# Kernel optimization log

Hardware: AMD Instinct MI355X
Metric: run time of the kernel (lower is better)

Reference implementation:

```python
import jax, jax.numpy as jnp
import numpy as np

B = 131072
EPS = 1e-5

def _attn(x, Wq, Wk, Wv, Wo):
    # x: (B, 10, 1); Wq/Wk/Wv: (1, 16); Wo: (16, 1)
    Q = x @ Wq  # (B, 10, 16)
    K = x @ Wk
    V = x @ Wv
    A = jnp.einsum('bqd,bkd->bqk', Q, K) / 4.0  # sqrt(16) = 4
    A = jax.nn.softmax(A, axis=1)  # NOTE: torch Softmax(dim=1) -> axis 1, not -1
    out = jnp.einsum('bqk,bkd->bqd', A, V) @ Wo  # (B, 10, 1)
    return out[..., 0]  # squeeze -> (B, 10)

def _bn(h, gamma, beta):
    # BatchNorm1d training-mode math (batch stats, biased variance)
    mu = jnp.mean(h, axis=0)
    var = jnp.mean(jnp.square(h - mu), axis=0)
    return gamma * (h - mu) * jax.lax.rsqrt(var + EPS) + beta

def setup_inputs() -> dict:
    key = jax.random.key(0)
    ks = jax.random.split(key, 24)
    n = lambda k, shp, s=1.0: (jax.random.normal(k, shp, dtype=jnp.float32) * s)
    inp = {
        'x':   n(ks[0], (B, 10, 1)),
        'Wq1': n(ks[1], (1, 16)), 'Wk1': n(ks[2], (1, 16)),
        'Wv1': n(ks[3], (1, 16)), 'Wo1': n(ks[4], (16, 1)),
        'Wq2': n(ks[5], (1, 16)), 'Wk2': n(ks[6], (1, 16)),
        'Wv2': n(ks[7], (1, 16)), 'Wo2': n(ks[8], (16, 1)),
        # layer1: Linear(10,128) BN ReLU Linear(128,256) BN ReLU Linear(256,10)
        'W1a': n(ks[9], (10, 128), 0.3), 'b1a': jnp.zeros((128,), jnp.float32),
        'g1a': jnp.ones((128,), jnp.float32), 'be1a': jnp.zeros((128,), jnp.float32),
        'W1b': n(ks[10], (128, 256), 0.09), 'b1b': jnp.zeros((256,), jnp.float32),
        'g1b': jnp.ones((256,), jnp.float32), 'be1b': jnp.zeros((256,), jnp.float32),
        'W1c': n(ks[11], (256, 10), 0.06), 'b1c': jnp.zeros((10,), jnp.float32),
        # layer2: Linear(10,128) BN ReLU Linear(128,256) BN ReLU Linear(256,2)
        'W2a': n(ks[12], (10, 128), 0.3), 'b2a': jnp.zeros((128,), jnp.float32),
        'g2a': jnp.ones((128,), jnp.float32), 'be2a': jnp.zeros((128,), jnp.float32),
        'W2b': n(ks[13], (128, 256), 0.09), 'b2b': jnp.zeros((256,), jnp.float32),
        'g2b': jnp.ones((256,), jnp.float32), 'be2b': jnp.zeros((256,), jnp.float32),
        'W2c': n(ks[14], (256, 2), 0.06), 'b2c': jnp.zeros((2,), jnp.float32),
    }
    return inp

def reference(x, Wq1, Wk1, Wv1, Wo1, Wq2, Wk2, Wv2, Wo2,
              W1a, b1a, g1a, be1a, W1b, b1b, g1b, be1b, W1c, b1c,
              W2a, b2a, g2a, be2a, W2b, b2b, g2b, be2b, W2c, b2c):
    h = _attn(x, Wq1, Wk1, Wv1, Wo1)                 # (B, 10)
    h = jax.nn.relu(_bn(h @ W1a + b1a, g1a, be1a))   # (B, 128)
    h = jax.nn.relu(_bn(h @ W1b + b1b, g1b, be1b))   # (B, 256)
    h = h @ W1c + b1c                                # (B, 10)
    h = _attn(h[..., None], Wq2, Wk2, Wv2, Wo2)      # (B, 10)
    h = jax.nn.relu(_bn(h @ W2a + b2a, g2a, be2a))   # (B, 128)
    h = jax.nn.relu(_bn(h @ W2b + b2b, g2b, be2b))   # (B, 256)
    return h @ W2c + b2c                             # (B, 2)
```

## Files before the change

kernel.cpp:

```cpp
#include <hip/hip_runtime.h>
#include <hip/hip_bf16.h>

#define EPS 1e-5f
constexpr int BN = 131072;
constexpr int NBKT = 32;
constexpr int NTILE = BN/64;
constexpr int TILE_ELEMS = 256*64;

typedef __attribute__((ext_vector_type(8))) short bf16x8;
typedef __attribute__((ext_vector_type(4))) float f32x4;

constexpr size_t OFF_H   = 0;
constexpr size_t OFF_HH  = OFF_H  + (size_t)BN*10;
constexpr size_t OFF_M1  = OFF_HH + (size_t)BN*10;
constexpr size_t OFF_S2  = OFF_M1 + 65;
constexpr size_t OFF_M3  = OFF_S2 + 512;
constexpr size_t OFF_S4  = OFF_M3 + 65;
constexpr size_t OFF_WA1 = OFF_S4 + 512;
constexpr size_t OFF_BA1 = OFF_WA1 + 1280;
constexpr size_t OFF_WA2 = OFF_BA1 + 128;
constexpr size_t OFF_BA2 = OFF_WA2 + 1280;
constexpr size_t OFF_SC2 = OFF_BA2 + 128;
constexpr size_t OFF_TC2 = OFF_SC2 + 256;
constexpr size_t OFF_SC4 = OFF_TC2 + 256;
constexpr size_t OFF_TC4 = OFF_SC4 + 256;
constexpr size_t OFF_WB1 = OFF_TC4 + 256;
constexpr size_t OFF_BB1 = OFF_WB1 + 32768;
constexpr size_t OFF_WB2 = OFF_BB1 + 256;
constexpr size_t OFF_BB2 = OFF_WB2 + 32768;
constexpr size_t OFF_P1  = OFF_BB2 + 256;
constexpr size_t OFF_P3  = OFF_P1 + 1024*65;
constexpr size_t OFF_S2B = OFF_P3 + 1024*65;
constexpr size_t OFF_S4B = OFF_S2B + (size_t)NBKT*512;
constexpr size_t OFF_WT1 = OFF_S4B + (size_t)NBKT*512;
constexpr size_t OFF_WT2 = OFF_WT1 + 16384;
constexpr size_t OFF_END = OFF_WT2 + 16384;
constexpr size_t OFF_Z_BYTES = ((OFF_END*4 + 255) & ~(size_t)255);
constexpr size_t WS_NEED = OFF_Z_BYTES + (size_t)NTILE*TILE_ELEMS*2;

__device__ __forceinline__ float wsum(float v){
  v += __shfl_down(v, 32);
  v += __shfl_down(v, 16);
  v += __shfl_down(v, 8);
  v += __shfl_down(v, 4);
  v += __shfl_down(v, 2);
  v += __shfl_down(v, 1);
  return v;
}

__device__ __forceinline__ unsigned pk_bf16(float a, float b){
  union { __hip_bfloat16 h[2]; unsigned u; } cv;
  cv.h[0] = __float2bfloat16(a);
  cv.h[1] = __float2bfloat16(b);
  return cv.u;
}

__device__ __forceinline__ unsigned short bf16_1(float a){
  union { __hip_bfloat16 h; unsigned short u; } cv;
  cv.h = __float2bfloat16(a);
  return cv.u;
}

__device__ __forceinline__ float bf16_to_f(unsigned short u){
  return __uint_as_float(((unsigned)u) << 16);
}

__device__ __forceinline__ void attn10(const float* xr, float cqk, float cvo, float* y){
  #pragma unroll
  for (int q=0;q<10;q++) y[q] = 0.f;
  #pragma unroll
  for (int k=0;k<10;k++){
    float t = cqk * xr[k];
    float m = t*xr[0];
    #pragma unroll
    for (int q=1;q<10;q++) m = fmaxf(m, t*xr[q]);
    float ex[10]; float s = 0.f;
    #pragma unroll
    for (int q=0;q<10;q++){ ex[q] = __expf(t*xr[q]-m); s += ex[q]; }
    float f = xr[k]/s;
    #pragma unroll
    for (int q=0;q<10;q++) y[q] += ex[q]*f;
  }
  #pragma unroll
  for (int q=0;q<10;q++) y[q] *= cvo;
}

__device__ __forceinline__ void moments_block(const float* y, float (*red)[65],
                                              float* Pb, int t){
  int lane = t & 63, w = t >> 6;
  #pragma unroll
  for (int i=0;i<10;i++){
    float v = wsum(y[i]);
    if (lane==0) red[w][i] = v;
  }
  #pragma unroll
  for (int i=0;i<10;i++){
    #pragma unroll
    for (int j=i;j<10;j++){
      float v = wsum(y[i]*y[j]);
      if (lane==0) red[w][10 + 10*i - i*(i-1)/2 + (j-i)] = v;
    }
  }
  __syncthreads();
  if (t < 65)
    Pb[(size_t)blockIdx.x*65 + t] = red[0][t]+red[1][t]+red[2][t]+red[3][t];
}

__device__ __forceinline__ void moments10(const float* y, float* M, int lane){
  #pragma unroll
  for (int i=0;i<10;i++){
    float s = wsum(y[i]);
    if (lane==0) atomicAdd(&M[i], s);
  }
  #pragma unroll
  for (int i=0;i<10;i++){
    #pragma unroll
    for (int j=i;j<10;j++){
      int id = 10*i - i*(i-1)/2 + (j-i);
      float s = wsum(y[i]*y[j]);
      if (lane==0) atomicAdd(&M[10+id], s);
    }
  }
}

__global__ __launch_bounds__(256) void k_attn_in(
    const float* __restrict__ x,
    const float* __restrict__ Wq, const float* __restrict__ Wk,
    const float* __restrict__ Wv, const float* __restrict__ Wo,
    float* __restrict__ h, float* __restrict__ Pb){
  __shared__ float xs[256][11];
  __shared__ float red[4][65];
  int t = threadIdx.x;
  size_t base = (size_t)blockIdx.x*2560;
  for (int idx=t; idx<2560; idx+=256) xs[idx/10][idx%10] = x[base+idx];
  float cqk=0.f, cvo=0.f;
  #pragma unroll
  for (int d=0;d<16;d++){ cqk += Wq[d]*Wk[d]; cvo += Wv[d]*Wo[d]; }
  cqk *= 0.25f;
  __syncthreads();
  float xr[10];
  #pragma unroll
  for (int q=0;q<10;q++) xr[q] = xs[t][q];
  float y[10];
  attn10(xr, cqk, cvo, y);
  #pragma unroll
  for (int q=0;q<10;q++) xs[t][q] = y[q];
  moments_block(y, red, Pb, t);
  for (int idx=t; idx<2560; idx+=256) h[base+idx] = xs[idx/10][idx%10];
}

__global__ void k_fold10_part(const float* __restrict__ Pb, int npart,
                              const float* __restrict__ W,
                              const float* __restrict__ bv, const float* __restrict__ g,
                              const float* __restrict__ be,
                              float* __restrict__ WT, float* __restrict__ bo){
  __shared__ float part[65][8];
  __shared__ float sM[65];
  int t = threadIdx.x;
  if (t < 520){
    int c = t>>3, k = t&7;
    int n = npart>>3;
    float acc = 0.f;
    #pragma unroll 4
    for (int i=0;i<n;i++) acc += Pb[(size_t)(k*n+i)*65 + c];
    part[c][k] = acc;
  }
  __syncthreads();
  if (t < 65){
    float a = 0.f;
    #pragma unroll
    for (int k=0;k<8;k++) a += part[t][k];
    sM[t] = a;
  }
  __syncthreads();
  int j = t;
  if (j >= 128) return;
  const float invB = 1.f/(float)BN;
  float Eh[10];
  #pragma unroll
  for (int i=0;i<10;i++) Eh[i] = sM[i]*invB;
  float wj[10];
  #pragma unroll
  for (int i=0;i<10;i++) wj[i] = W[i*128+j];
  float mu = bv[j];
  #pragma unroll
  for (int i=0;i<10;i++) mu += Eh[i]*wj[i];
  float var = 0.f;
  #pragma unroll
  for (int i=0;i<10;i++){
    #pragma unroll
    for (int l=0;l<10;l++){
      int a = i<l ? i : l, c = i<l ? l : i;
      int id = 10*a - a*(a-1)/2 + (c-a);
      float cov = sM[10+id]*invB - Eh[i]*Eh[l];
      var += wj[i]*wj[l]*cov;
    }
  }
  float s = g[j]*rsqrtf(var + EPS);
  #pragma unroll
  for (int i=0;i<10;i++) WT[j*10+i] = wj[i]*s;
  bo[j] = (bv[j]-mu)*s + be[j];
}

__global__ void k_fold10_atomic(const float* __restrict__ M,
                                const float* __restrict__ W,
                                const float* __restrict__ bv, const float* __restrict__ g,
                                const float* __restrict__ be,
                                float* __restrict__ WT, float* __restrict__ bo){
  int j = threadIdx.x;
  if (j >= 128) return;
  const float invB = 1.f/(float)BN;
  float Eh[10];
  #pragma unroll
  for (int i=0;i<10;i++) Eh[i] = M[i]*invB;
  float wj[10];
  #pragma unroll
  for (int i=0;i<10;i++) wj[i] = W[i*128+j];
  float mu = bv[j];
  #pragma unroll
  for (int i=0;i<10;i++) mu += Eh[i]*wj[i];
  float var = 0.f;
  #pragma unroll
  for (int i=0;i<10;i++){
    #pragma unroll
    for (int l=0;l<10;l++){
      int a = i<l ? i : l, c = i<l ? l : i;
      int id = 10*a - a*(a-1)/2 + (c-a);
      float cov = M[10+id]*invB - Eh[i]*Eh[l];
      var += wj[i]*wj[l]*cov;
    }
  }
  float s = g[j]*rsqrtf(var + EPS);
  #pragma unroll
  for (int i=0;i<10;i++) WT[j*10+i] = wj[i]*s;
  bo[j] = (bv[j]-mu)*s + be[j];
}

__global__ void k_fold_affine(const float* __restrict__ stats,
                              const float* __restrict__ g,
                              const float* __restrict__ be,
                              float* __restrict__ s, float* __restrict__ tt){
  int j = threadIdx.x;
  if (j >= 256) return;
  float su = 0.f, sq = 0.f;
  #pragma unroll 4
  for (int k=0;k<NBKT;k++){
    su += stats[k*512 + j];
    sq += stats[k*512 + 256 + j];
  }
  const float invB = 1.f/(float)BN;
  float mu  = su*invB;
  float var = sq*invB - mu*mu;
  float sc = g[j]*rsqrtf(var + EPS);
  s[j]  = sc;
  tt[j] = be[j] - mu*sc;
}

__global__ __launch_bounds__(256) void k_prep_wt2(
    const float* __restrict__ W1, const float* __restrict__ W2,
    unsigned short* __restrict__ WT1, unsigned short* __restrict__ WT2){
  int g = blockIdx.x;
  const float* W = (g < 128) ? W1 : W2;
  unsigned short* WT = (g < 128) ? WT1 : WT2;
  int idx = (g & 127)*256 + threadIdx.x;
  int c = idx >> 7, k = idx & 127;
  WT[idx] = bf16_1(W[k*256 + c]);
}

__global__ __launch_bounds__(256) void k_layer_mfma(
    const float* __restrict__ h,
    const float* __restrict__ WaT,
    const float* __restrict__ ba,
    const unsigned short* __restrict__ WT,
    const float* __restrict__ bb,
    unsigned short* __restrict__ zt,
    float* __restrict__ stats)
{
  __shared__ unsigned short h1s[2][64*128];
  __shared__ float hs[128][11];
  __shared__ float sWaT[1280];
  int t = threadIdx.x;
  int lane = t & 63, w = t >> 6;
  int ci = lane & 15, g = lane >> 4;
  size_t row0 = (size_t)blockIdx.x * 128;

  bf16x8 bfr[4][4];
  #pragma unroll
  for (int nt=0; nt<4; nt++)
    #pragma unroll
    for (int kt=0; kt<4; kt++){
      union { uint4 u; bf16x8 v; } cv;
      cv.u = *(const uint4*)(WT + (size_t)(w*64 + nt*16 + ci)*128 + kt*32 + g*8);
      bfr[nt][kt] = cv.v;
    }

  for (int idx = t; idx < 1280; idx += 256) hs[idx/10][idx%10] = h[row0*10 + idx];
  for (int idx = t; idx < 1280; idx += 256) sWaT[idx] = WaT[idx];
  __syncthreads();

  float bbv[4];
  #pragma unroll
  for (int nt=0;nt<4;nt++) bbv[nt] = bb[w*64 + nt*16 + ci];
  float cs[4] = {0,0,0,0}, cq[4] = {0,0,0,0};

  {
    int r = lane;
    int i0 = w * 32;
    float hr[10];
    #pragma unroll
    for (int l=0;l<10;l++) hr[l] = hs[r][l];
    #pragma unroll
    for (int j=0;j<4;j++){
      unsigned pk[4];
      #pragma unroll
      for (int q=0;q<4;q++){
        int i = i0 + j*8 + q*2;
        float v0 = ba[i], v1 = ba[i+1];
        #pragma unroll
        for (int l=0;l<10;l++){
          v0 = fmaf(hr[l], sWaT[i*10+l],     v0);
          v1 = fmaf(hr[l], sWaT[(i+1)*10+l], v1);
        }
        pk[q] = pk_bf16(fmaxf(v0,0.f), fmaxf(v1,0.f));
      }
      int byte = r*256 + (((i0 + j*8)*2) ^ ((r&7)<<4));
      *(uint4*)((char*)h1s[0] + byte) = make_uint4(pk[0],pk[1],pk[2],pk[3]);
    }
  }
  __syncthreads();

  f32x4 acc[4][4];
  #pragma unroll
  for (int mt=0;mt<4;mt++)
    #pragma unroll
    for (int nt=0;nt<4;nt++)
      acc[mt][nt] = (f32x4){0.f,0.f,0.f,0.f};
  #pragma unroll
  for (int mt=0; mt<4; mt++){
    int r = mt*16 + ci;
    bf16x8 af[4];
    #pragma unroll
    for (int kt=0; kt<4; kt++){
      int byte = r*256 + ((kt*64 + g*16) ^ ((r&7)<<4));
      af[kt] = *(const bf16x8*)((const char*)h1s[0] + byte);
    }
    #pragma unroll
    for (int nt=0; nt<4; nt++)
      #pragma unroll
      for (int kt=0; kt<4; kt++)
        acc[mt][nt] = __builtin_amdgcn_mfma_f32_16x16x32_bf16(
            af[kt], bfr[nt][kt], acc[mt][nt], 0, 0, 0);
  }

  {
    size_t tbase = ((size_t)blockIdx.x*2 + 0) * TILE_ELEMS;
    #pragma unroll
    for (int nt=0; nt<4; nt++){
      int c = w*64 + nt*16 + ci;
      #pragma unroll
      for (int mt=0; mt<4; mt++){
        float z0 = acc[mt][nt][0] + bbv[nt];
        float z1 = acc[mt][nt][1] + bbv[nt];
        float z2 = acc[mt][nt][2] + bbv[nt];
        float z3 = acc[mt][nt][3] + bbv[nt];
        cs[nt] += z0+z1+z2+z3;
        cq[nt] += z0*z0+z1*z1+z2*z2+z3*z3;
        *(uint2*)(zt + tbase + c*64 + mt*16 + g*4) =
            make_uint2(pk_bf16(z0,z1), pk_bf16(z2,z3));
      }
    }
  }

  {
    int r = lane;
    int i0 = w * 32;
    float hr[10];
    #pragma unroll
    for (int l=0;l<10;l++) hr[l] = hs[64 + r][l];
    #pragma unroll
    for (int j=0;j<4;j++){
      unsigned pk[4];
      #pragma unroll
      for (int q=0;q<4;q++){
        int i = i0 + j*8 + q*2;
        float v0 = ba[i], v1 = ba[i+1];
        #pragma unroll
        for (int l=0;l<10;l++){
          v0 = fmaf(hr[l], sWaT[i*10+l],     v0);
          v1 = fmaf(hr[l], sWaT[(i+1)*10+l], v1);
        }
        pk[q] = pk_bf16(fmaxf(v0,0.f), fmaxf(v1,0.f));
      }
      int byte = r*256 + (((i0 + j*8)*2) ^ ((r&7)<<4));
      *(uint4*)((char*)h1s[1] + byte) = make_uint4(pk[0],pk[1],pk[2],pk[3]);
    }
  }
  __syncthreads();

  #pragma unroll
  for (int mt=0;mt<4;mt++)
    #pragma unroll
    for (int nt=0;nt<4;nt++)
      acc[mt][nt] = (f32x4){0.f,0.f,0.f,0.f};
  #pragma unroll
  for (int mt=0; mt<4; mt++){
    int r = mt*16 + ci;
    bf16x8 af[4];
    #pragma unroll
    for (int kt=0; kt<4; kt++){
      int byte = r*256 + ((kt*64 + g*16) ^ ((r&7)<<4));
      af[kt] = *(const bf16x8*)((const char*)h1s[1] + byte);
    }
    #pragma unroll
    for (int nt=0; nt<4; nt++)
      #pragma unroll
      for (int kt=0; kt<4; kt++)
        acc[mt][nt] = __builtin_amdgcn_mfma_f32_16x16x32_bf16(
            af[kt], bfr[nt][kt], acc[mt][nt], 0, 0, 0);
  }

  {
    size_t tbase = ((size_t)blockIdx.x*2 + 1) * TILE_ELEMS;
    #pragma unroll
    for (int nt=0; nt<4; nt++){
      int c = w*64 + nt*16 + ci;
      #pragma unroll
      for (int mt=0; mt<4; mt++){
        float z0 = acc[mt][nt][0] + bbv[nt];
        float z1 = acc[mt][nt][1] + bbv[nt];
        float z2 = acc[mt][nt][2] + bbv[nt];
        float z3 = acc[mt][nt][3] + bbv[nt];
        cs[nt] += z0+z1+z2+z3;
        cq[nt] += z0*z0+z1*z1+z2*z2+z3*z3;
        *(uint2*)(zt + tbase + c*64 + mt*16 + g*4) =
            make_uint2(pk_bf16(z0,z1), pk_bf16(z2,z3));
      }
    }
  }

  #pragma unroll
  for (int nt=0; nt<4; nt++){
    float s1 = cs[nt], s2 = cq[nt];
    s1 += __shfl_down(s1, 32); s1 += __shfl_down(s1, 16);
    s2 += __shfl_down(s2, 32); s2 += __shfl_down(s2, 16);
    if (lane < 16){
      int bkt = blockIdx.x & (NBKT-1);
      int c = w*64 + nt*16 + ci;
      atomicAdd(&stats[bkt*512 + c],       s1);
      atomicAdd(&stats[bkt*512 + 256 + c], s2);
    }
  }
}

__global__ __launch_bounds__(256) void k_consume_mid(
    const unsigned short* __restrict__ zt,
    const float* __restrict__ s_g, const float* __restrict__ t_g,
    const float* __restrict__ Wc,  const float* __restrict__ bc,
    const float* __restrict__ Wq, const float* __restrict__ Wk,
    const float* __restrict__ Wv, const float* __restrict__ Wo,
    float* __restrict__ hh, float* __restrict__ Pb){
  __shared__ __align__(16) unsigned short zs[2][32*256];
  __shared__ __align__(16) float sWc[256*12];
  __shared__ float ss[256], st[256];
  __shared__ float red[4][65];
  int t = threadIdx.x;
  for (int idx=t; idx<2560; idx+=256) sWc[(idx/10)*12 + (idx%10)] = Wc[idx];
  ss[t] = s_g[t]; st[t] = t_g[t];
  size_t b0 = (size_t)blockIdx.x*256;

  float z3[10];
  #pragma unroll
  for (int l=0;l<10;l++) z3[l] = bc[l];

  int q = t >> 6, l = t & 63;
  size_t src_base = ((size_t)blockIdx.x*4 + q)*TILE_ELEMS + l*32;
  int dst_off = (l>>1)*256 + q*64 + (l&1)*32;
  uint4 r0, r1, r2, r3;
  {
    const uint4* src = (const uint4*)(zt + src_base);
    r0 = src[0]; r1 = src[1]; r2 = src[2]; r3 = src[3];
    uint4* dst = (uint4*)&zs[0][dst_off];
    dst[0] = r0; dst[1] = r1; dst[2] = r2; dst[3] = r3;
  }
  for (int cc=0; cc<8; cc++){
    __syncthreads();
    if (cc < 7){
      const uint4* src = (const uint4*)(zt + src_base + (size_t)(cc+1)*2048);
      r0 = src[0]; r1 = src[1]; r2 = src[2]; r3 = src[3];
    }
    const unsigned short* zb = zs[cc&1];
    #pragma unroll 4
    for (int cl=0; cl<32; cl++){
      int c = cc*32 + cl;
      float f = bf16_to_f(zb[cl*256 + t]);
      float h2 = fmaxf(fmaf(ss[c], f, st[c]), 0.f);
      const float4* wr = (const float4*)&sWc[c*12];
      float4 w0 = wr[0];
      float4 w1 = wr[1];
      float2 w2 = *(const float2*)&sWc[c*12 + 8];
      z3[0] = fmaf(h2, w0.x, z3[0]); z3[1] = fmaf(h2, w0.y, z3[1]);
      z3[2] = fmaf(h2, w0.z, z3[2]); z3[3] = fmaf(h2, w0.w, z3[3]);
      z3[4] = fmaf(h2, w1.x, z3[4]); z3[5] = fmaf(h2, w1.y, z3[5]);
      z3[6] = fmaf(h2, w1.z, z3[6]); z3[7] = fmaf(h2, w1.w, z3[7]);
      z3[8] = fmaf(h2, w2.x, z3[8]); z3[9] = fmaf(h2, w2.y, z3[9]);
    }
    if (cc < 7){
      uint4* dst = (uint4*)&zs[(cc+1)&1][dst_off];
      dst[0] = r0; dst[1] = r1; dst[2] = r2; dst[3] = r3;
    }
  }

  float cqk=0.f, cvo=0.f;
  #pragma unroll
  for (int d=0;d<16;d++){ cqk += Wq[d]*Wk[d]; cvo += Wv[d]*Wo[d]; }
  cqk *= 0.25f;
  float y[10];
  attn10(z3, cqk, cvo, y);
  __syncthreads();
  float* hhs = (float*)zs[0];
  #pragma unroll
  for (int qq=0;qq<10;qq++) hhs[t*10+qq] = y[qq];
  moments_block(y, red, Pb, t);
  for (int idx=t; idx<2560; idx+=256)
    hh[b0*10 + idx] = hhs[idx];
}

__global__ __launch_bounds__(256) void k_consume_out(
    const unsigned short* __restrict__ zt,
    const float* __restrict__ s_g, const float* __restrict__ t_g,
    const float* __restrict__ Wc,  const float* __restrict__ bc,
    float* __restrict__ out){
  __shared__ __align__(16) unsigned short zs[2][32*256];
  __shared__ __align__(8) float sWo[512];
  __shared__ float ss[256], st[256];
  int t = threadIdx.x;
  sWo[t] = Wc[t]; sWo[256+t] = Wc[256+t];
  ss[t] = s_g[t]; st[t] = t_g[t];
  size_t b0 = (size_t)blockIdx.x*256;
  float o0 = bc[0], o1 = bc[1];
  int q = t >> 6, l = t & 63;
  size_t src_base = ((size_t)blockIdx.x*4 + q)*TILE_ELEMS + l*32;
  int dst_off = (l>>1)*256 + q*64 + (l&1)*32;
  uint4 r0, r1, r2, r3;
  {
    const uint4* src = (const uint4*)(zt + src_base);
    r0 = src[0]; r1 = src[1]; r2 = src[2]; r3 = src[3];
    uint4* dst = (uint4*)&zs[0][dst_off];
    dst[0] = r0; dst[1] = r1; dst[2] = r2; dst[3] = r3;
  }
  for (int cc=0; cc<8; cc++){
    __syncthreads();
    if (cc < 7){
      const uint4* src = (const uint4*)(zt + src_base + (size_t)(cc+1)*2048);
      r0 = src[0]; r1 = src[1]; r2 = src[2]; r3 = src[3];
    }
    const unsigned short* zb = zs[cc&1];
    #pragma unroll 8
    for (int cl=0; cl<32; cl++){
      int c = cc*32 + cl;
      float f = bf16_to_f(zb[cl*256 + t]);
      float h5 = fmaxf(fmaf(ss[c], f, st[c]), 0.f);
      float2 wv = *(const float2*)&sWo[c*2];
      o0 = fmaf(h5, wv.x, o0);
      o1 = fmaf(h5, wv.y, o1);
    }
    if (cc < 7){
      uint4* dst = (uint4*)&zs[(cc+1)&1][dst_off];
      dst[0] = r0; dst[1] = r1; dst[2] = r2; dst[3] = r3;
    }
  }
  *(float2*)(out + (b0 + t)*2) = make_float2(o0, o1);
}

__global__ void k_fold_big(const float* __restrict__ stats,
                           const float* __restrict__ W,
                           const float* __restrict__ bv, const float* __restrict__ g,
                           const float* __restrict__ be,
                           float* __restrict__ Wf, float* __restrict__ bf){
  int j = blockIdx.x*256 + threadIdx.x;
  if (j >= 256) return;
  const float invB = 1.f/(float)BN;
  float mu  = stats[j]*invB;
  float var = stats[256+j]*invB - mu*mu;
  float s = g[j]*rsqrtf(var + EPS);
  bf[j] = (bv[j]-mu)*s + be[j];
  for (int i=0;i<128;i++) Wf[i*256+j] = W[i*256+j]*s;
}

__global__ __launch_bounds__(256) void k_mid(
    const float* __restrict__ h,
    const float* __restrict__ WaT, const float* __restrict__ ba,
    const float* __restrict__ Wb,  const float* __restrict__ bb,
    float* __restrict__ stats){
  int b = blockIdx.x*256 + threadIdx.x;
  if (b >= BN) return;
  float hr[10];
  #pragma unroll
  for (int l=0;l<10;l++) hr[l] = h[(size_t)b*10+l];
  int lane = threadIdx.x & 63;
  for (int jc=0;jc<4;jc++){
    float acc[64];
    #pragma unroll
    for (int j=0;j<64;j++) acc[j] = bb[jc*64+j];
    for (int i=0;i<128;i++){
      float h1 = ba[i];
      #pragma unroll
      for (int l=0;l<10;l++) h1 += hr[l]*WaT[i*10+l];
      h1 = fmaxf(h1, 0.f);
      const float* __restrict__ w = &Wb[i*256 + jc*64];
      #pragma unroll
      for (int j=0;j<64;j++) acc[j] += h1*w[j];
    }
    #pragma unroll
    for (int j=0;j<64;j++){
      float s1 = wsum(acc[j]);
      float s2 = wsum(acc[j]*acc[j]);
      if (lane==0){
        atomicAdd(&stats[jc*64+j], s1);
        atomicAdd(&stats[256+jc*64+j], s2);
      }
    }
  }
}

__global__ __launch_bounds__(256) void k_mid2(
    const float* __restrict__ h,
    const float* __restrict__ WaT, const float* __restrict__ ba,
    const float* __restrict__ Wbf, const float* __restrict__ bbf,
    const float* __restrict__ Wc,  const float* __restrict__ bc,
    const float* __restrict__ Wq, const float* __restrict__ Wk,
    const float* __restrict__ Wv, const float* __restrict__ Wo,
    float* __restrict__ hh, float* __restrict__ M){
  int b = blockIdx.x*256 + threadIdx.x;
  if (b >= BN) return;
  float hr[10];
  #pragma unroll
  for (int l=0;l<10;l++) hr[l] = h[(size_t)b*10+l];
  float z3[10];
  #pragma unroll
  for (int l=0;l<10;l++) z3[l] = bc[l];
  for (int jc=0;jc<4;jc++){
    float acc[64];
    #pragma unroll
    for (int j=0;j<64;j++) acc[j] = bbf[jc*64+j];
    for (int i=0;i<128;i++){
      float h1 = ba[i];
      #pragma unroll
      for (int l=0;l<10;l++) h1 += hr[l]*WaT[i*10+l];
      h1 = fmaxf(h1, 0.f);
      const float* __restrict__ w = &Wbf[i*256 + jc*64];
      #pragma unroll
      for (int j=0;j<64;j++) acc[j] += h1*w[j];
    }
    #pragma unroll
    for (int j=0;j<64;j++){
      float h2 = fmaxf(acc[j], 0.f);
      const float* __restrict__ wc = &Wc[(jc*64+j)*10];
      #pragma unroll
      for (int l=0;l<10;l++) z3[l] += h2*wc[l];
    }
  }
  float cqk=0.f, cvo=0.f;
  #pragma unroll
  for (int d=0;d<16;d++){ cqk += Wq[d]*Wk[d]; cvo += Wv[d]*Wo[d]; }
  cqk *= 0.25f;
  float y[10];
  attn10(z3, cqk, cvo, y);
  #pragma unroll
  for (int q=0;q<10;q++) hh[(size_t)b*10+q] = y[q];
  moments10(y, M, threadIdx.x & 63);
}

__global__ __launch_bounds__(256) void k_out(
    const float* __restrict__ h,
    const float* __restrict__ WaT, const float* __restrict__ ba,
    const float* __restrict__ Wbf, const float* __restrict__ bbf,
    const float* __restrict__ Wc,  const float* __restrict__ bc,
    float* __restrict__ out){
  int b = blockIdx.x*256 + threadIdx.x;
  if (b >= BN) return;
  float hr[10];
  #pragma unroll
  for (int l=0;l<10;l++) hr[l] = h[(size_t)b*10+l];
  float o0 = bc[0], o1 = bc[1];
  for (int jc=0;jc<4;jc++){
    float acc[64];
    #pragma unroll
    for (int j=0;j<64;j++) acc[j] = bbf[jc*64+j];
    for (int i=0;i<128;i++){
      float h4 = ba[i];
      #pragma unroll
      for (int l=0;l<10;l++) h4 += hr[l]*WaT[i*10+l];
      h4 = fmaxf(h4, 0.f);
      const float* __restrict__ w = &Wbf[i*256 + jc*64];
      #pragma unroll
      for (int j=0;j<64;j++) acc[j] += h4*w[j];
    }
    #pragma unroll
    for (int j=0;j<64;j++){
      float h5 = fmaxf(acc[j], 0.f);
      o0 += h5*Wc[(jc*64+j)*2];
      o1 += h5*Wc[(jc*64+j)*2+1];
    }
  }
  out[(size_t)b*2]   = o0;
  out[(size_t)b*2+1] = o1;
}

extern "C" void kernel_launch(void* const* d_in, const int* in_sizes, int n_in,
                              void* d_out, int out_size, void* d_ws, size_t ws_size,
                              hipStream_t stream){
  const float* x   = (const float*)d_in[0];
  const float* Wq1 = (const float*)d_in[1];
  const float* Wk1 = (const float*)d_in[2];
  const float* Wv1 = (const float*)d_in[3];
  const float* Wo1 = (const float*)d_in[4];
  const float* Wq2 = (const float*)d_in[5];
  const float* Wk2 = (const float*)d_in[6];
  const float* Wv2 = (const float*)d_in[7];
  const float* Wo2 = (const float*)d_in[8];
  const float* W1a = (const float*)d_in[9];  const float* b1a = (const float*)d_in[10];
  const float* g1a = (const float*)d_in[11]; const float* be1a= (const float*)d_in[12];
  const float* W1b = (const float*)d_in[13]; const float* b1b = (const float*)d_in[14];
  const float* g1b = (const float*)d_in[15]; const float* be1b= (const float*)d_in[16];
  const float* W1c = (const float*)d_in[17]; const float* b1c = (const float*)d_in[18];
  const float* W2a = (const float*)d_in[19]; const float* b2a = (const float*)d_in[20];
  const float* g2a = (const float*)d_in[21]; const float* be2a= (const float*)d_in[22];
  const float* W2b = (const float*)d_in[23]; const float* b2b = (const float*)d_in[24];
  const float* g2b = (const float*)d_in[25]; const float* be2b= (const float*)d_in[26];
  const float* W2c = (const float*)d_in[27]; const float* b2c = (const float*)d_in[28];

  float* f   = (float*)d_ws;
  float* h   = f + OFF_H;
  float* hh  = f + OFF_HH;
  float* M1  = f + OFF_M1;
  float* S2  = f + OFF_S2;
  float* M3  = f + OFF_M3;
  float* S4  = f + OFF_S4;
  float* WA1 = f + OFF_WA1; float* BA1 = f + OFF_BA1;
  float* WA2 = f + OFF_WA2; float* BA2 = f + OFF_BA2;
  float* SC2 = f + OFF_SC2; float* TC2 = f + OFF_TC2;
  float* SC4 = f + OFF_SC4; float* TC4 = f + OFF_TC4;
  float* WB1 = f + OFF_WB1; float* BB1 = f + OFF_BB1;
  float* WB2 = f + OFF_WB2; float* BB2 = f + OFF_BB2;
  float* P1  = f + OFF_P1;  float* P3  = f + OFF_P3;
  float* S2B = f + OFF_S2B; float* S4B = f + OFF_S4B;
  unsigned short* WT1 = (unsigned short*)(f + OFF_WT1);
  unsigned short* WT2 = (unsigned short*)(f + OFF_WT2);
  unsigned short* ZT = (unsigned short*)((char*)d_ws + OFF_Z_BYTES);

  dim3 blk(256);
  dim3 grid256(BN/256);
  dim3 grid128(BN/128);

  if (ws_size >= WS_NEED){
    hipMemsetAsync(S2B, 0, (size_t)2*NBKT*512*sizeof(float), stream);
    k_prep_wt2<<<256,blk,0,stream>>>(W1b, W2b, WT1, WT2);
    k_attn_in<<<grid256,blk,0,stream>>>(x, Wq1,Wk1,Wv1,Wo1, h, P1);
    k_fold10_part<<<1,576,0,stream>>>(P1, 512, W1a,b1a,g1a,be1a, WA1,BA1);
    k_layer_mfma<<<grid128,blk,0,stream>>>(h, WA1,BA1, WT1,b1b, ZT, S2B);
    k_fold_affine<<<1,256,0,stream>>>(S2B, g1b, be1b, SC2, TC2);
    k_consume_mid<<<grid256,blk,0,stream>>>(ZT, SC2,TC2, W1c,b1c,
                                            Wq2,Wk2,Wv2,Wo2, hh, P3);
    k_fold10_part<<<1,576,0,stream>>>(P3, 512, W2a,b2a,g2a,be2a, WA2,BA2);
    k_layer_mfma<<<grid128,blk,0,stream>>>(hh, WA2,BA2, WT2,b2b, ZT, S4B);
    k_fold_affine<<<1,256,0,stream>>>(S4B, g2b, be2b, SC4, TC4);
    k_consume_out<<<grid256,blk,0,stream>>>(ZT, SC4,TC4, W2c,b2c, (float*)d_out);
  } else {
    hipMemsetAsync(M1, 0, (65+512+65+512)*sizeof(float), stream);
    k_attn_in<<<grid256,blk,0,stream>>>(x, Wq1,Wk1,Wv1,Wo1, h, P1);
    k_fold10_part<<<1,576,0,stream>>>(P1, 512, W1a,b1a,g1a,be1a, WA1,BA1);
    k_mid<<<grid256,blk,0,stream>>>(h, WA1,BA1, W1b,b1b, S2);
    k_fold_big<<<1,256,0,stream>>>(S2, W1b,b1b,g1b,be1b, WB1,BB1);
    k_mid2<<<grid256,blk,0,stream>>>(h, WA1,BA1, WB1,BB1, W1c,b1c,
                                     Wq2,Wk2,Wv2,Wo2, hh, M3);
    k_fold10_atomic<<<1,128,0,stream>>>(M3, W2a,b2a,g2a,be2a, WA2,BA2);
    k_mid<<<grid256,blk,0,stream>>>(hh, WA2,BA2, W2b,b2b, S4);
    k_fold_big<<<1,256,0,stream>>>(S4, W2b,b2b,g2b,be2b, WB2,BB2);
    k_out<<<grid256,blk,0,stream>>>(hh, WA2,BA2, WB2,BB2, W2c,b2c, (float*)d_out);
  }
}
```

Baseline: 207.8 us.

## Process two rows per thread in consume kernels with swizzled single-buffer LDS

The two consumer kernels now handle 512 rows per block, two per thread. Each thread reads a packed pair of bf16 values with one 32-bit LDS load, so the same scale, shift and weight loads serve two rows. The double-buffered staging is replaced by a single XOR-swizzled LDS buffer and eight-vector register prefetch, with an extra barrier per chunk. This halves the grid and changes the partial-moment count passed to the fold kernel, in exchange for more registers per thread and fewer blocks to spread across the device.

```diff
diff --git a/kernel.cpp b/kernel.cpp
--- a/kernel.cpp
+++ b/kernel.cpp
@@ -64,6 +64,8 @@
 __device__ __forceinline__ float bf16_to_f(unsigned short u){
   return __uint_as_float(((unsigned)u) << 16);
 }
+__device__ __forceinline__ float bf16_lo(unsigned u){ return __uint_as_float(u << 16); }
+__device__ __forceinline__ float bf16_hi(unsigned u){ return __uint_as_float(u & 0xffff0000u); }
 
 __device__ __forceinline__ void attn10(const float* xr, float cqk, float cvo, float* y){
   #pragma unroll
@@ -459,54 +461,61 @@
     const float* __restrict__ Wq, const float* __restrict__ Wk,
     const float* __restrict__ Wv, const float* __restrict__ Wo,
     float* __restrict__ hh, float* __restrict__ Pb){
-  __shared__ __align__(16) unsigned short zs[2][32*256];
+  __shared__ __align__(16) unsigned short zs[32*512];
   __shared__ __align__(16) float sWc[256*12];
   __shared__ float ss[256], st[256];
   __shared__ float red[4][65];
   int t = threadIdx.x;
   for (int idx=t; idx<2560; idx+=256) sWc[(idx/10)*12 + (idx%10)] = Wc[idx];
   ss[t] = s_g[t]; st[t] = t_g[t];
-  size_t b0 = (size_t)blockIdx.x*256;
-
-  float z3[10];
-  #pragma unroll
-  for (int l=0;l<10;l++) z3[l] = bc[l];
-
-  int q = t >> 6, l = t & 63;
-  size_t src_base = ((size_t)blockIdx.x*4 + q)*TILE_ELEMS + l*32;
-  int dst_off = (l>>1)*256 + q*64 + (l&1)*32;
-  uint4 r0, r1, r2, r3;
+  size_t b0 = (size_t)blockIdx.x*512;
+
+  float z3a[10], z3b[10];
+  #pragma unroll
+  for (int l=0;l<10;l++){ z3a[l] = bc[l]; z3b[l] = bc[l]; }
+
+  int q8 = t >> 5, cl0 = t & 31;
+  size_t src_base = ((size_t)blockIdx.x*8 + q8)*TILE_ELEMS + (size_t)cl0*64;
+  int sbits = (cl0 & 7) << 4;
+  char* wbase = (char*)zs + cl0*1024;
+
+  uint4 pf[8];
   {
-    const uint4* src = (const uint4*)(zt + src_base);
-    r0 = src[0]; r1 = src[1]; r2 = src[2]; r3 = src[3];
-    uint4* dst = (uint4*)&zs[0][dst_off];
-    dst[0] = r0; dst[1] = r1; dst[2] = r2; dst[3] = r3;
+    const uint4* s = (const uint4*)(zt + src_base);
+    #pragma unroll
+    for (int k=0;k<8;k++) pf[k] = s[k];
   }
   for (int cc=0; cc<8; cc++){
     __syncthreads();
+    #pragma unroll
+    for (int k=0;k<8;k++)
+      *(uint4*)(wbase + ((q8*128 + k*16) ^ sbits)) = pf[k];
     if (cc < 7){
-      const uint4* src = (const uint4*)(zt + src_base + (size_t)(cc+1)*2048);
-      r0 = src[0]; r1 = src[1]; r2 = src[2]; r3 = src[3];
-    }
-    const unsigned short* zb = zs[cc&1];
+      const uint4* s = (const uint4*)(zt + src_base + (size_t)(cc+1)*2048);
+      #pragma unroll
+      for (int k=0;k<8;k++) pf[k] = s[k];
+    }
+    __syncthreads();
     #pragma unroll 4
     for (int cl=0; cl<32; cl++){
       int c = cc*32 + cl;
-      float f = bf16_to_f(zb[cl*256 + t]);
-      float h2 = fmaxf(fmaf(ss[c], f, st[c]), 0.f);
+      unsigned u = *(const unsigned*)((const char*)zs + cl*1024 + ((4*t) ^ ((cl&7)<<4)));
+      float ha = fmaxf(fmaf(ss[c], bf16_lo(u), st[c]), 0.f);
+      float hb = fmaxf(fmaf(ss[c], bf16_hi(u), st[c]), 0.f);
       const float4* wr = (const float4*)&sWc[c*12];
       float4 w0 = wr[0];
       float4 w1 = wr[1];
       float2 w2 = *(const float2*)&sWc[c*12 + 8];
-      z3[0] = fmaf(h2, w0.x, z3[0]); z3[1] = fmaf(h2, w0.y, z3[1]);
-      z3[2] = fmaf(h2, w0.z, z3[2]); z3[3] = fmaf(h2, w0.w, z3[3]);
-      z3[4] = fmaf(h2, w1.x, z3[4]); z3[5] = fmaf(h2, w1.y, z3[5]);
-      z3[6] = fmaf(h2, w1.z, z3[6]); z3[7] = fmaf(h2, w1.w, z3[7]);
-      z3[8] = fmaf(h2, w2.x, z3[8]); z3[9] = fmaf(h2, w2.y, z3[9]);
-    }
-    if (cc < 7){
-      uint4* dst = (uint4*)&zs[(cc+1)&1][dst_off];
-      dst[0] = r0; dst[1] = r1; dst[2] = r2; dst[3] = r3;
+      z3a[0]=fmaf(ha,w0.x,z3a[0]); z3b[0]=fmaf(hb,w0.x,z3b[0]);
+      z3a[1]=fmaf(ha,w0.y,z3a[1]); z3b[1]=fmaf(hb,w0.y,z3b[1]);
+      z3a[2]=fmaf(ha,w0.z,z3a[2]); z3b[2]=fmaf(hb,w0.z,z3b[2]);
+      z3a[3]=fmaf(ha,w0.w,z3a[3]); z3b[3]=fmaf(hb,w0.w,z3b[3]);
+      z3a[4]=fmaf(ha,w1.x,z3a[4]); z3b[4]=fmaf(hb,w1.x,z3b[4]);
+      z3a[5]=fmaf(ha,w1.y,z3a[5]); z3b[5]=fmaf(hb,w1.y,z3b[5]);
+      z3a[6]=fmaf(ha,w1.z,z3a[6]); z3b[6]=fmaf(hb,w1.z,z3b[6]);
+      z3a[7]=fmaf(ha,w1.w,z3a[7]); z3b[7]=fmaf(hb,w1.w,z3b[7]);
+      z3a[8]=fmaf(ha,w2.x,z3a[8]); z3b[8]=fmaf(hb,w2.x,z3b[8]);
+      z3a[9]=fmaf(ha,w2.y,z3a[9]); z3b[9]=fmaf(hb,w2.y,z3b[9]);
     }
   }
 
@@ -514,14 +523,35 @@
   #pragma unroll
   for (int d=0;d<16;d++){ cqk += Wq[d]*Wk[d]; cvo += Wv[d]*Wo[d]; }
   cqk *= 0.25f;
-  float y[10];
-  attn10(z3, cqk, cvo, y);
+  float ya[10], yb[10];
+  attn10(z3a, cqk, cvo, ya);
+  attn10(z3b, cqk, cvo, yb);
+
   __syncthreads();
-  float* hhs = (float*)zs[0];
-  #pragma unroll
-  for (int qq=0;qq<10;qq++) hhs[t*10+qq] = y[qq];
-  moments_block(y, red, Pb, t);
-  for (int idx=t; idx<2560; idx+=256)
+  float* hhs = (float*)zs;
+  #pragma unroll
+  for (int q=0;q<10;q++){ hhs[(2*t)*10+q] = ya[q]; hhs[(2*t+1)*10+q] = yb[q]; }
+
+  {
+    int lane = t & 63, w = t >> 6;
+    #pragma unroll
+    for (int i=0;i<10;i++){
+      float v = wsum(ya[i] + yb[i]);
+      if (lane==0) red[w][i] = v;
+    }
+    #pragma unroll
+    for (int i=0;i<10;i++){
+      #pragma unroll
+      for (int j=i;j<10;j++){
+        float v = wsum(ya[i]*ya[j] + yb[i]*yb[j]);
+        if (lane==0) red[w][10 + 10*i - i*(i-1)/2 + (j-i)] = v;
+      }
+    }
+  }
+  __syncthreads();
+  if (t < 65)
+    Pb[(size_t)blockIdx.x*65 + t] = red[0][t]+red[1][t]+red[2][t]+red[3][t];
+  for (int idx=t; idx<5120; idx+=256)
     hh[b0*10 + idx] = hhs[idx];
 }
 
@@ -530,46 +560,48 @@
     const float* __restrict__ s_g, const float* __restrict__ t_g,
     const float* __restrict__ Wc,  const float* __restrict__ bc,
     float* __restrict__ out){
-  __shared__ __align__(16) unsigned short zs[2][32*256];
+  __shared__ __align__(16) unsigned short zs[32*512];
   __shared__ __align__(8) float sWo[512];
   __shared__ float ss[256], st[256];
   int t = threadIdx.x;
   sWo[t] = Wc[t]; sWo[256+t] = Wc[256+t];
   ss[t] = s_g[t]; st[t] = t_g[t];
-  size_t b0 = (size_t)blockIdx.x*256;
-  float o0 = bc[0], o1 = bc[1];
-  int q = t >> 6, l = t & 63;
-  size_t src_base = ((size_t)blockIdx.x*4 + q)*TILE_ELEMS + l*32;
-  int dst_off = (l>>1)*256 + q*64 + (l&1)*32;
-  uint4 r0, r1, r2, r3;
+  size_t b0 = (size_t)blockIdx.x*512;
+  float o0a = bc[0], o1a = bc[1];
+  float o0b = bc[0], o1b = bc[1];
+  int q8 = t >> 5, cl0 = t & 31;
+  size_t src_base = ((size_t)blockIdx.x*8 + q8)*TILE_ELEMS + (size_t)cl0*64;
+  int sbits = (cl0 & 7) << 4;
+  char* wbase = (char*)zs + cl0*1024;
+  uint4 pf[8];
   {
-    const uint4* src = (const uint4*)(zt + src_base);
-    r0 = src[0]; r1 = src[1]; r2 = src[2]; r3 = src[3];
-    uint4* dst = (uint4*)&zs[0][dst_off];
-    dst[0] = r0; dst[1] = r1; dst[2] = r2; dst[3] = r3;
+    const uint4* s = (const uint4*)(zt + src_base);
+    #pragma unroll
+    for (int k=0;k<8;k++) pf[k] = s[k];
   }
   for (int cc=0; cc<8; cc++){
     __syncthreads();
+    #pragma unroll
+    for (int k=0;k<8;k++)
+      *(uint4*)(wbase + ((q8*128 + k*16) ^ sbits)) = pf[k];
     if (cc < 7){
-      const uint4* src = (const uint4*)(zt + src_base + (size_t)(cc+1)*2048);
-      r0 = src[0]; r1 = src[1]; r2 = src[2]; r3 = src[3];
-    }
-    const unsigned short* zb = zs[cc&1];
+      const uint4* s = (const uint4*)(zt + src_base + (size_t)(cc+1)*2048);
+      #pragma unroll
+      for (int k=0;k<8;k++) pf[k] = s[k];
+    }
+    __syncthreads();
     #pragma unroll 8
     for (int cl=0; cl<32; cl++){
       int c = cc*32 + cl;
-      float f = bf16_to_f(zb[cl*256 + t]);
-      float h5 = fmaxf(fmaf(ss[c], f, st[c]), 0.f);
+      unsigned u = *(const unsigned*)((const char*)zs + cl*1024 + ((4*t) ^ ((cl&7)<<4)));
+      float ha = fmaxf(fmaf(ss[c], bf16_lo(u), st[c]), 0.f);
+      float hb = fmaxf(fmaf(ss[c], bf16_hi(u), st[c]), 0.f);
       float2 wv = *(const float2*)&sWo[c*2];
-      o0 = fmaf(h5, wv.x, o0);
-      o1 = fmaf(h5, wv.y, o1);
-    }
-    if (cc < 7){
-      uint4* dst = (uint4*)&zs[(cc+1)&1][dst_off];
-      dst[0] = r0; dst[1] = r1; dst[2] = r2; dst[3] = r3;
-    }
-  }
-  *(float2*)(out + (b0 + t)*2) = make_float2(o0, o1);
+      o0a = fmaf(ha, wv.x, o0a); o1a = fmaf(ha, wv.y, o1a);
+      o0b = fmaf(hb, wv.x, o0b); o1b = fmaf(hb, wv.y, o1b);
+    }
+  }
+  *(float4*)(out + (b0 + 2*t)*2) = make_float4(o0a, o1a, o0b, o1b);
 }
 
 __global__ void k_fold_big(const float* __restrict__ stats,
@@ -752,6 +784,7 @@
   dim3 blk(256);
   dim3 grid256(BN/256);
   dim3 grid128(BN/128);
+  dim3 grid512(BN/512);
 
   if (ws_size >= WS_NEED){
     hipMemsetAsync(S2B, 0, (size_t)2*NBKT*512*sizeof(float), stream);
@@ -760,12 +793,12 @@
     k_fold10_part<<<1,576,0,stream>>>(P1, 512, W1a,b1a,g1a,be1a, WA1,BA1);
     k_layer_mfma<<<grid128,blk,0,stream>>>(h, WA1,BA1, WT1,b1b, ZT, S2B);
     k_fold_affine<<<1,256,0,stream>>>(S2B, g1b, be1b, SC2, TC2);
-    k_consume_mid<<<grid256,blk,0,stream>>>(ZT, SC2,TC2, W1c,b1c,
+    k_consume_mid<<<grid512,blk,0,stream>>>(ZT, SC2,TC2, W1c,b1c,
                                             Wq2,Wk2,Wv2,Wo2, hh, P3);
-    k_fold10_part<<<1,576,0,stream>>>(P3, 512, W2a,b2a,g2a,be2a, WA2,BA2);
+    k_fold10_part<<<1,576,0,stream>>>(P3, 256, W2a,b2a,g2a,be2a, WA2,BA2);
     k_layer_mfma<<<grid128,blk,0,stream>>>(hh, WA2,BA2, WT2,b2b, ZT, S4B);
     k_fold_affine<<<1,256,0,stream>>>(S4B, g2b, be2b, SC4, TC4);
-    k_consume_out<<<grid256,blk,0,stream>>>(ZT, SC4,TC4, W2c,b2c, (float*)d_out);
+    k_consume_out<<<grid512,blk,0,stream>>>(ZT, SC4,TC4, W2c,b2c, (float*)d_out);
   } else {
     hipMemsetAsync(M1, 0, (65+512+65+512)*sizeof(float), stream);
     k_attn_in<<<grid256,blk,0,stream>>>(x, Wq1,Wk1,Wv1,Wo1, h, P1);
```

Measured after the change: 233.7 us. +12.5%, slower.
